# Optimization experiments

Hardware: AMD Instinct MI355X
Metric: run time of the kernel (lower is better)

Reference implementation:

```python
import jax, jax.numpy as jnp
import numpy as np


def setup_inputs() -> dict:
    key = jax.random.key(0)
    k1, k2 = jax.random.split(key)
    B, S, H, E = 4, 8192, 4096, 64
    x = jax.random.normal(k1, (B, S, H), dtype=jnp.float32)
    # gate weight [E, H], scaled like a standard init_method
    weight = jax.random.normal(k2, (E, H), dtype=jnp.float32) * (H ** -0.5)
    expert_biases = jnp.zeros((E,), dtype=jnp.float32)
    return {"x": x, "weight": weight, "expert_biases": expert_biases, "top_k": 8}


def reference(x, weight, expert_biases, top_k):
    BIAS_UPDATE_RATE = 0.01
    batch_shape = x.shape[:-1]
    E, H = weight.shape
    flat_x = x.reshape(-1, H)            # [N, H]
    n_tokens = flat_x.shape[0]

    raw_scores = flat_x @ weight.T       # [N, E] gate GEMM
    probs = jax.nn.softmax(raw_scores + expert_biases, axis=-1)  # biased softmax

    expert_weights, expert_indices = jax.lax.top_k(probs, top_k)  # [N, K]

    # bincount with fixed length E (jit-friendly scatter-add)
    token_counts = jnp.zeros((E,), jnp.int32).at[expert_indices.reshape(-1)].add(1)

    # loss-free balancing bias update (training-time buffer update)
    tokens_per_expert = n_tokens * top_k / E
    load_violations = token_counts.astype(jnp.float32) - tokens_per_expert
    new_expert_biases = expert_biases + BIAS_UPDATE_RATE * jnp.sign(load_violations)

    scores = probs.reshape(*batch_shape, E)
    expert_weights = expert_weights.reshape(*batch_shape, top_k)
    expert_indices = expert_indices.reshape(*batch_shape, top_k)
    return (scores, expert_weights, expert_indices, new_expert_biases)
```

## Files before the change

kernel.cpp:

```cpp
#include <hip/hip_runtime.h>

#define NE 64
#define TAU 1e-4f
#define LSTR 68

typedef __bf16 bf16x8 __attribute__((ext_vector_type(8)));
typedef float f32x4 __attribute__((ext_vector_type(4)));

__device__ __forceinline__ void split8(const float4 a0, const float4 a1,
                                       bf16x8& hi, bf16x8& lo) {
  const float xs[8] = {a0.x, a0.y, a0.z, a0.w, a1.x, a1.y, a1.z, a1.w};
#pragma unroll
  for (int i = 0; i < 8; ++i) {
    const __bf16 h = (__bf16)xs[i];
    hi[i] = h;
    lo[i] = (__bf16)(xs[i] - (float)h);
  }
}

__device__ __forceinline__ void gld16(const void* g, void* l) {
  __builtin_amdgcn_global_load_lds(
      (const __attribute__((address_space(1))) void*)g,
      (__attribute__((address_space(3))) void*)l, 16, 0, 0);
}

__global__ void zero512(int* __restrict__ p) { p[threadIdx.x] = 0; }

__global__ __launch_bounds__(256) void wconvert(const float* __restrict__ W,
                                                __bf16* __restrict__ Whi,
                                                __bf16* __restrict__ Wlo,
                                                int n8, int H) {
  const int i = blockIdx.x * 256 + threadIdx.x;
  if (i >= n8) return;
  const int hc = H >> 3;
  const int e = i / hc;
  const int k0 = (i - e * hc) * 8;
  const float4 a0 = *reinterpret_cast<const float4*>(W + (size_t)e * H + k0);
  const float4 a1 =
      *reinterpret_cast<const float4*>(W + (size_t)e * H + k0 + 4);
  bf16x8 hi, lo;
  split8(a0, a1, hi, lo);
  const int tt = k0 >> 5, lk = (k0 >> 3) & 3, j = e >> 4, lr = e & 15;
  const size_t off = (size_t)tt * 2048 + j * 512 + (lk * 16 + lr) * 8;
  *reinterpret_cast<bf16x8*>(Whi + off) = hi;
  *reinterpret_cast<bf16x8*>(Wlo + off) = lo;
}

template <int BUF>
__device__ __forceinline__ void issue_tile(int t, const float* const (&srcA)[4],
                                           const __bf16* srcBh,
                                           const __bf16* srcBl, char* smem,
                                           int wave) {
  float* af = (float*)(smem) + BUF * 4096;
  __bf16* bh = (__bf16*)(smem + 32768) + BUF * 4096;
  __bf16* bl = (__bf16*)(smem + 49152) + BUF * 4096;
#pragma unroll
  for (int p = 0; p < 4; ++p)
    gld16(srcA[p] + 64 * (size_t)t, af + wave * 1024 + p * 256);
  gld16(srcBh + 4096 * (size_t)t, bh + wave * 512);
  gld16(srcBh + 4096 * (size_t)t + 2048, bh + 2048 + wave * 512);
  gld16(srcBl + 4096 * (size_t)t, bl + wave * 512);
  gld16(srcBl + 4096 * (size_t)t + 2048, bl + 2048 + wave * 512);
}

template <int BUF>
__device__ __forceinline__ void compute_tile(char* smem, int wave, int lane,
                                             int lr, int lk, int swz,
                                             f32x4 (&acc)[4]) {
  const float* Aw = (float*)(smem) + BUF * 4096 + wave * 1024 + lr * 64;
  const __bf16* Bh0 = (__bf16*)(smem + 32768) + BUF * 4096;
  const __bf16* Bl0 = (__bf16*)(smem + 49152) + BUF * 4096;
#pragma unroll
  for (int kk = 0; kk < 2; ++kk) {
    const int c = 8 * kk + 2 * lk;
    const float4 f0 = *reinterpret_cast<const float4*>(Aw + 4 * (c ^ swz));
    const float4 f1 =
        *reinterpret_cast<const float4*>(Aw + 4 * ((c + 1) ^ swz));
    bf16x8 Ahi, Alo;
    split8(f0, f1, Ahi, Alo);
    const __bf16* Bh = Bh0 + kk * 2048;
    const __bf16* Bl = Bl0 + kk * 2048;
    bf16x8 BH[4], BL[4];
#pragma unroll
    for (int j = 0; j < 4; ++j) {
      BH[j] = *reinterpret_cast<const bf16x8*>(Bh + j * 512 + lane * 8);
      BL[j] = *reinterpret_cast<const bf16x8*>(Bl + j * 512 + lane * 8);
    }
#pragma unroll
    for (int j = 0; j < 4; ++j)
      acc[j] = __builtin_amdgcn_mfma_f32_16x16x32_bf16(Alo, BL[j], acc[j], 0, 0, 0);
#pragma unroll
    for (int j = 0; j < 4; ++j)
      acc[j] = __builtin_amdgcn_mfma_f32_16x16x32_bf16(Alo, BH[j], acc[j], 0, 0, 0);
#pragma unroll
    for (int j = 0; j < 4; ++j)
      acc[j] = __builtin_amdgcn_mfma_f32_16x16x32_bf16(Ahi, BL[j], acc[j], 0, 0, 0);
#pragma unroll
    for (int j = 0; j < 4; ++j)
      acc[j] = __builtin_amdgcn_mfma_f32_16x16x32_bf16(Ahi, BH[j], acc[j], 0, 0, 0);
  }
}

__global__ __launch_bounds__(256, 2) void gemm_fused(
    const float* __restrict__ X, const __bf16* __restrict__ Whi,
    const __bf16* __restrict__ Wlo, const float* __restrict__ bias,
    float* __restrict__ S, float* __restrict__ wout, float* __restrict__ iout,
    int* __restrict__ cnt, int* __restrict__ hist, int* __restrict__ list,
    int cap, int H, int K) {
  __shared__ alignas(16) char smem[65536];
  __shared__ int hist_s[NE];
  const int tid = threadIdx.x;
  const int lane = tid & 63;
  const int wave = tid >> 6;
  if (tid < NE) hist_s[tid] = 0;
  const int lr = lane & 15;
  const int lk = lane >> 4;
  const int row0 = blockIdx.x * 64;

  const float* srcA[4];
#pragma unroll
  for (int p = 0; p < 4; ++p) {
    const int rr = 4 * p + (lane >> 4);
    const int sp = lane & 15;
    srcA[p] = X + (size_t)(row0 + 16 * wave + rr) * H + 4 * (sp ^ (rr & 7));
  }
  const __bf16* srcBh = Whi + wave * 512 + lane * 8;
  const __bf16* srcBl = Wlo + wave * 512 + lane * 8;

  f32x4 acc[4] = {};
  const int T2 = H / 64;
  const int swz = lr & 7;

  issue_tile<0>(0, srcA, srcBh, srcBl, smem, wave);
  for (int t = 0; t < T2; t += 2) {
    if (t + 1 < T2) {
      issue_tile<1>(t + 1, srcA, srcBh, srcBl, smem, wave);
      asm volatile("s_waitcnt vmcnt(8)" ::: "memory");
    } else {
      asm volatile("s_waitcnt vmcnt(0)" ::: "memory");
    }
    __builtin_amdgcn_s_barrier();
    asm volatile("" ::: "memory");
    compute_tile<0>(smem, wave, lane, lr, lk, swz, acc);
    asm volatile("" ::: "memory");
    __builtin_amdgcn_s_barrier();
    asm volatile("" ::: "memory");
    if (t + 2 < T2) {
      issue_tile<0>(t + 2, srcA, srcBh, srcBl, smem, wave);
      asm volatile("s_waitcnt vmcnt(8)" ::: "memory");
    } else {
      asm volatile("s_waitcnt vmcnt(0)" ::: "memory");
    }
    __builtin_amdgcn_s_barrier();
    asm volatile("" ::: "memory");
    compute_tile<1>(smem, wave, lane, lr, lk, swz, acc);
    asm volatile("" ::: "memory");
    __builtin_amdgcn_s_barrier();
    asm volatile("" ::: "memory");
  }

  float* Ls = (float*)smem;
#pragma unroll
  for (int j = 0; j < 4; ++j)
#pragma unroll
    for (int r = 0; r < 4; ++r)
      Ls[(16 * wave + 4 * lk + r) * LSTR + 16 * j + lr] = acc[j][r];
  __syncthreads();

  const float bv = bias[lane];
  for (int tt = 0; tt < 16; ++tt) {
    const int tl = wave * 16 + tt;
    const int t = row0 + tl;
    const float s = Ls[tl * LSTR + lane] + bv;

    float m = s;
#pragma unroll
    for (int off = 32; off >= 1; off >>= 1) m = fmaxf(m, __shfl_xor(m, off));
    const float e = expf(s - m);
    float sum = e;
#pragma unroll
    for (int off = 32; off >= 1; off >>= 1) sum += __shfl_xor(sum, off);
    const float p = e / sum;

    float wsel = s;
    float rv = 0.f;
    int ri = 0;
    float prev = 0.f, mingap = 1e30f;
#pragma unroll
    for (int r = 0; r < 9; ++r) {
      float v = wsel;
      int ii = lane;
#pragma unroll
      for (int off = 32; off >= 1; off >>= 1) {
        const float ov = __shfl_xor(v, off);
        const int oi = __shfl_xor(ii, off);
        if (ov > v || (ov == v && oi < ii)) { v = ov; ii = oi; }
      }
      if (r > 0) mingap = fminf(mingap, prev - v);
      prev = v;
      const float pw = __shfl(p, ii);
      if (lane == r) { rv = pw; ri = ii; }
      if (lane == ii) wsel = -1e30f;
    }

    bool toC = false;
    if (mingap < TAU && cap > 0) {
      int pos = 0;
      if (lane == 0) pos = atomicAdd(cnt, 1);
      pos = __shfl(pos, 0);
      if (pos < cap) {
        if (lane == 0) list[pos] = t;
        toC = true;
      }
    }
    if (!toC) {
      S[(size_t)t * NE + lane] = p;
      if (lane < K) {
        wout[(size_t)t * K + lane] = rv;
        iout[(size_t)t * K + lane] = (float)ri;
        atomicAdd(&hist_s[ri], 1);
      }
    }
  }
  __syncthreads();
  if (tid < NE) atomicAdd(&hist[tid], hist_s[tid]);
}

__device__ __forceinline__ void finalize_token_f64(
    int t, int lane, double s, float* __restrict__ S, float* __restrict__ wout,
    float* __restrict__ iout, int* __restrict__ hist, int K) {
  double m = s;
#pragma unroll
  for (int off = 32; off >= 1; off >>= 1) m = fmax(m, __shfl_xor(m, off));
  const double ex = exp(s - m);
  double sum = ex;
#pragma unroll
  for (int off = 32; off >= 1; off >>= 1) sum += __shfl_xor(sum, off);
  const double p = ex / sum;
  S[(size_t)t * NE + lane] = (float)p;
  double wsel = s;
  double rv = 0.0;
  int ri = 0;
  for (int r = 0; r < K; ++r) {
    double v = wsel;
    int ii = lane;
#pragma unroll
    for (int off = 32; off >= 1; off >>= 1) {
      const double ov = __shfl_xor(v, off);
      const int oi = __shfl_xor(ii, off);
      if (ov > v || (ov == v && oi < ii)) { v = ov; ii = oi; }
    }
    const double pw = __shfl(p, ii);
    if (lane == r) { rv = pw; ri = ii; }
    if (lane == ii) wsel = -1e300;
  }
  if (lane < K) {
    wout[(size_t)t * K + lane] = (float)rv;
    iout[(size_t)t * K + lane] = (float)ri;
    atomicAdd(&hist[ri], 1);
  }
}

__global__ __launch_bounds__(256) void recompute_f64(
    const float* __restrict__ X, const float* __restrict__ W,
    const float* __restrict__ bias, float* __restrict__ S,
    float* __restrict__ wout, float* __restrict__ iout,
    const int* __restrict__ cnt, const int* __restrict__ list,
    int* __restrict__ hist, int H, int K, int cap) {
  if (cap <= 0) return;
  __shared__ float4 xs[1024];
  __shared__ double red[256];
  const int tid = threadIdx.x;
  const int n = min(*cnt, cap);
  const int H4 = H >> 2;
  for (int idx = blockIdx.x; idx < n; idx += gridDim.x) {
    const int t = list[idx];
    __syncthreads();
    const float4* xg = reinterpret_cast<const float4*>(X + (size_t)t * H);
    for (int i = tid; i < H4; i += 256) xs[i] = xg[i];
    __syncthreads();
    const int e = tid & 63, sl = tid >> 6;
    const int seg = H4 >> 2;
    const float4* wr =
        reinterpret_cast<const float4*>(W + (size_t)e * H) + (size_t)sl * seg;
    const float4* xr = &xs[sl * seg];
    double a0 = 0.0, a1 = 0.0;
    for (int k = 0; k < seg; k += 2) {
      const float4 w0 = wr[k], w1 = wr[k + 1];
      const float4 v0 = xr[k], v1 = xr[k + 1];
      a0 = fma((double)v0.x, (double)w0.x, a0);
      a0 = fma((double)v0.y, (double)w0.y, a0);
      a0 = fma((double)v0.z, (double)w0.z, a0);
      a0 = fma((double)v0.w, (double)w0.w, a0);
      a1 = fma((double)v1.x, (double)w1.x, a1);
      a1 = fma((double)v1.y, (double)w1.y, a1);
      a1 = fma((double)v1.z, (double)w1.z, a1);
      a1 = fma((double)v1.w, (double)w1.w, a1);
    }
    red[tid] = a0 + a1;
    __syncthreads();
    if (tid < 64) {
      const double s =
          red[e] + red[64 + e] + red[128 + e] + red[192 + e] + (double)bias[e];
      finalize_token_f64(t, e, s, S, wout, iout, hist, K);
    }
  }
}

__global__ void bias_update(const int* __restrict__ hist,
                            const float* __restrict__ bias,
                            float* __restrict__ bout, float tpe) {
  const int e = threadIdx.x;
  const float d = (float)hist[e] - tpe;
  const float sg = (d > 0.f) ? 1.f : ((d < 0.f) ? -1.f : 0.f);
  bout[e] = bias[e] + 0.01f * sg;
}

extern "C" void kernel_launch(void* const* d_in, const int* in_sizes, int n_in,
                              void* d_out, int out_size, void* d_ws, size_t ws_size,
                              hipStream_t stream) {
  const float* x = (const float*)d_in[0];
  const float* w = (const float*)d_in[1];
  const float* bias = (const float*)d_in[2];
  const int E = in_sizes[2];
  const int H = in_sizes[1] / E;
  const long long N = (long long)in_sizes[0] / H;
  const int K = (int)(((long long)out_size - N * E - E) / (2 * N));

  float* S = (float*)d_out;
  float* wout = S + (size_t)N * E;
  float* iout = wout + (size_t)N * K;
  float* bout = iout + (size_t)N * K;

  int* cnt = (int*)d_ws;
  int* hist = (int*)d_ws + 64;
  const size_t whalf = (size_t)E * H * sizeof(__bf16);
  __bf16* Whi = (__bf16*)((char*)d_ws + 4096);
  __bf16* Wlo = (__bf16*)((char*)d_ws + 4096 + whalf);
  const size_t listoff = 4096 + 2 * whalf;
  int* list = (int*)((char*)d_ws + listoff);
  int cap = 0;
  if (ws_size > listoff + 65536)
    cap = (int)min((size_t)32768, (ws_size - listoff) / 4);

  zero512<<<dim3(1), dim3(128), 0, stream>>>((int*)d_ws);
  const int n8 = E * H / 8;
  wconvert<<<dim3((n8 + 255) / 256), 256, 0, stream>>>(w, Whi, Wlo, n8, H);
  gemm_fused<<<dim3((int)(N / 64)), 256, 0, stream>>>(
      x, Whi, Wlo, bias, S, wout, iout, cnt, hist, list, cap, H, K);
  recompute_f64<<<dim3(512), 256, 0, stream>>>(x, w, bias, S, wout, iout, cnt,
                                               list, hist, H, K, cap);
  bias_update<<<dim3(1), dim3(E), 0, stream>>>(hist, bias, bout,
                                               (float)((double)N * K / E));
}
```

Measured before the change: 285.9 us.

## Split gate GEMM K-dimension in two and move softmax/top-k to separate kernel

```diff
diff --git a/kernel.cpp b/kernel.cpp
--- a/kernel.cpp
+++ b/kernel.cpp
@@ -47,118 +47,110 @@
 }
 
 template <int BUF>
-__device__ __forceinline__ void issue_tile(int t, const float* const (&srcA)[4],
+__device__ __forceinline__ void issue_tile(int t, const float* srcA0,
+                                           const float* srcA1,
                                            const __bf16* srcBh,
                                            const __bf16* srcBl, char* smem,
                                            int wave) {
-  float* af = (float*)(smem) + BUF * 4096;
-  __bf16* bh = (__bf16*)(smem + 32768) + BUF * 4096;
-  __bf16* bl = (__bf16*)(smem + 49152) + BUF * 4096;
-#pragma unroll
-  for (int p = 0; p < 4; ++p)
-    gld16(srcA[p] + 64 * (size_t)t, af + wave * 1024 + p * 256);
-  gld16(srcBh + 4096 * (size_t)t, bh + wave * 512);
-  gld16(srcBh + 4096 * (size_t)t + 2048, bh + 2048 + wave * 512);
-  gld16(srcBl + 4096 * (size_t)t, bl + wave * 512);
-  gld16(srcBl + 4096 * (size_t)t + 2048, bl + 2048 + wave * 512);
+  float* af = (float*)smem + BUF * 2048;
+  __bf16* bh = (__bf16*)(smem + 16384) + BUF * 2048;
+  __bf16* bl = (__bf16*)(smem + 24576) + BUF * 2048;
+  gld16(srcA0 + 32 * (size_t)t, af + wave * 512);
+  gld16(srcA1 + 32 * (size_t)t, af + wave * 512 + 256);
+  gld16(srcBh + 2048 * (size_t)t, bh + wave * 512);
+  gld16(srcBl + 2048 * (size_t)t, bl + wave * 512);
 }
 
 template <int BUF>
 __device__ __forceinline__ void compute_tile(char* smem, int wave, int lane,
-                                             int lr, int lk, int swz,
-                                             f32x4 (&acc)[4]) {
-  const float* Aw = (float*)(smem) + BUF * 4096 + wave * 1024 + lr * 64;
-  const __bf16* Bh0 = (__bf16*)(smem + 32768) + BUF * 4096;
-  const __bf16* Bl0 = (__bf16*)(smem + 49152) + BUF * 4096;
-#pragma unroll
-  for (int kk = 0; kk < 2; ++kk) {
-    const int c = 8 * kk + 2 * lk;
-    const float4 f0 = *reinterpret_cast<const float4*>(Aw + 4 * (c ^ swz));
-    const float4 f1 =
-        *reinterpret_cast<const float4*>(Aw + 4 * ((c + 1) ^ swz));
-    bf16x8 Ahi, Alo;
-    split8(f0, f1, Ahi, Alo);
-    const __bf16* Bh = Bh0 + kk * 2048;
-    const __bf16* Bl = Bl0 + kk * 2048;
-    bf16x8 BH[4], BL[4];
-#pragma unroll
-    for (int j = 0; j < 4; ++j) {
-      BH[j] = *reinterpret_cast<const bf16x8*>(Bh + j * 512 + lane * 8);
-      BL[j] = *reinterpret_cast<const bf16x8*>(Bl + j * 512 + lane * 8);
-    }
-#pragma unroll
-    for (int j = 0; j < 4; ++j)
-      acc[j] = __builtin_amdgcn_mfma_f32_16x16x32_bf16(Alo, BL[j], acc[j], 0, 0, 0);
-#pragma unroll
-    for (int j = 0; j < 4; ++j)
-      acc[j] = __builtin_amdgcn_mfma_f32_16x16x32_bf16(Alo, BH[j], acc[j], 0, 0, 0);
-#pragma unroll
-    for (int j = 0; j < 4; ++j)
-      acc[j] = __builtin_amdgcn_mfma_f32_16x16x32_bf16(Ahi, BL[j], acc[j], 0, 0, 0);
-#pragma unroll
-    for (int j = 0; j < 4; ++j)
-      acc[j] = __builtin_amdgcn_mfma_f32_16x16x32_bf16(Ahi, BH[j], acc[j], 0, 0, 0);
-  }
-}
-
-__global__ __launch_bounds__(256, 2) void gemm_fused(
+                                             int lr, int lk, f32x4 (&acc)[4]) {
+  const float* Aw = (float*)smem + BUF * 2048 + wave * 512 + (lr >> 3) * 256 +
+                    (lr & 7) * 32;
+  const int s0 = (2 * lk) ^ (lr & 7);
+  const int s1 = (2 * lk + 1) ^ (lr & 7);
+  const float4 f0 = *reinterpret_cast<const float4*>(Aw + s0 * 4);
+  const float4 f1 = *reinterpret_cast<const float4*>(Aw + s1 * 4);
+  const __bf16* Bh0 = (__bf16*)(smem + 16384) + BUF * 2048;
+  const __bf16* Bl0 = (__bf16*)(smem + 24576) + BUF * 2048;
+  bf16x8 BHf[4], BLf[4];
+#pragma unroll
+  for (int j = 0; j < 4; ++j) {
+    BHf[j] = *reinterpret_cast<const bf16x8*>(Bh0 + j * 512 + lane * 8);
+    BLf[j] = *reinterpret_cast<const bf16x8*>(Bl0 + j * 512 + lane * 8);
+  }
+  bf16x8 Ahi, Alo;
+  split8(f0, f1, Ahi, Alo);
+#pragma unroll
+  for (int j = 0; j < 4; ++j)
+    acc[j] = __builtin_amdgcn_mfma_f32_16x16x32_bf16(Alo, BLf[j], acc[j], 0, 0, 0);
+#pragma unroll
+  for (int j = 0; j < 4; ++j)
+    acc[j] = __builtin_amdgcn_mfma_f32_16x16x32_bf16(Alo, BHf[j], acc[j], 0, 0, 0);
+#pragma unroll
+  for (int j = 0; j < 4; ++j)
+    acc[j] = __builtin_amdgcn_mfma_f32_16x16x32_bf16(Ahi, BLf[j], acc[j], 0, 0, 0);
+#pragma unroll
+  for (int j = 0; j < 4; ++j)
+    acc[j] = __builtin_amdgcn_mfma_f32_16x16x32_bf16(Ahi, BHf[j], acc[j], 0, 0, 0);
+}
+
+__global__ __launch_bounds__(256, 4) void gemm_half(
     const float* __restrict__ X, const __bf16* __restrict__ Whi,
-    const __bf16* __restrict__ Wlo, const float* __restrict__ bias,
-    float* __restrict__ S, float* __restrict__ wout, float* __restrict__ iout,
-    int* __restrict__ cnt, int* __restrict__ hist, int* __restrict__ list,
-    int cap, int H, int K) {
-  __shared__ alignas(16) char smem[65536];
-  __shared__ int hist_s[NE];
+    const __bf16* __restrict__ Wlo, float* __restrict__ S0,
+    float* __restrict__ P2, int H) {
+  __shared__ alignas(16) char smem[32768];
   const int tid = threadIdx.x;
   const int lane = tid & 63;
   const int wave = tid >> 6;
-  if (tid < NE) hist_s[tid] = 0;
   const int lr = lane & 15;
   const int lk = lane >> 4;
   const int row0 = blockIdx.x * 64;
-
-  const float* srcA[4];
-#pragma unroll
-  for (int p = 0; p < 4; ++p) {
-    const int rr = 4 * p + (lane >> 4);
-    const int sp = lane & 15;
-    srcA[p] = X + (size_t)(row0 + 16 * wave + rr) * H + 4 * (sp ^ (rr & 7));
-  }
-  const __bf16* srcBh = Whi + wave * 512 + lane * 8;
-  const __bf16* srcBl = Wlo + wave * 512 + lane * 8;
+  const int kbeg = blockIdx.y * (H >> 1);
+  float* __restrict__ P = blockIdx.y ? P2 : S0;
+
+  const int rr0 = lane >> 3;
+  const int sp = lane & 7;
+  const float* srcA0 =
+      X + (size_t)(row0 + 16 * wave + rr0) * H + kbeg + 4 * (sp ^ rr0);
+  const float* srcA1 =
+      X + (size_t)(row0 + 16 * wave + 8 + rr0) * H + kbeg + 4 * (sp ^ rr0);
+  const __bf16* srcBh =
+      Whi + (size_t)(blockIdx.y * 64) * 2048 + wave * 512 + lane * 8;
+  const __bf16* srcBl =
+      Wlo + (size_t)(blockIdx.y * 64) * 2048 + wave * 512 + lane * 8;
 
   f32x4 acc[4] = {};
-  const int T2 = H / 64;
-  const int swz = lr & 7;
-
-  issue_tile<0>(0, srcA, srcBh, srcBl, smem, wave);
+  const int T2 = H >> 6;
+
+  issue_tile<0>(0, srcA0, srcA1, srcBh, srcBl, smem, wave);
   for (int t = 0; t < T2; t += 2) {
     if (t + 1 < T2) {
-      issue_tile<1>(t + 1, srcA, srcBh, srcBl, smem, wave);
-      asm volatile("s_waitcnt vmcnt(8)" ::: "memory");
+      issue_tile<1>(t + 1, srcA0, srcA1, srcBh, srcBl, smem, wave);
+      asm volatile("s_waitcnt vmcnt(4)" ::: "memory");
     } else {
       asm volatile("s_waitcnt vmcnt(0)" ::: "memory");
     }
     __builtin_amdgcn_s_barrier();
     asm volatile("" ::: "memory");
-    compute_tile<0>(smem, wave, lane, lr, lk, swz, acc);
+    compute_tile<0>(smem, wave, lane, lr, lk, acc);
     asm volatile("" ::: "memory");
     __builtin_amdgcn_s_barrier();
     asm volatile("" ::: "memory");
     if (t + 2 < T2) {
-      issue_tile<0>(t + 2, srcA, srcBh, srcBl, smem, wave);
-      asm volatile("s_waitcnt vmcnt(8)" ::: "memory");
+      issue_tile<0>(t + 2, srcA0, srcA1, srcBh, srcBl, smem, wave);
+      asm volatile("s_waitcnt vmcnt(4)" ::: "memory");
     } else {
       asm volatile("s_waitcnt vmcnt(0)" ::: "memory");
     }
     __builtin_amdgcn_s_barrier();
     asm volatile("" ::: "memory");
-    compute_tile<1>(smem, wave, lane, lr, lk, swz, acc);
+    compute_tile<1>(smem, wave, lane, lr, lk, acc);
     asm volatile("" ::: "memory");
     __builtin_amdgcn_s_barrier();
     asm volatile("" ::: "memory");
   }
 
+  __syncthreads();
   float* Ls = (float*)smem;
 #pragma unroll
   for (int j = 0; j < 4; ++j)
@@ -166,12 +158,30 @@
     for (int r = 0; r < 4; ++r)
       Ls[(16 * wave + 4 * lk + r) * LSTR + 16 * j + lr] = acc[j][r];
   __syncthreads();
-
-  const float bv = bias[lane];
   for (int tt = 0; tt < 16; ++tt) {
     const int tl = wave * 16 + tt;
-    const int t = row0 + tl;
-    const float s = Ls[tl * LSTR + lane] + bv;
+    P[(size_t)(row0 + tl) * NE + lane] = Ls[tl * LSTR + lane];
+  }
+}
+
+__global__ __launch_bounds__(256) void finish(
+    const float* __restrict__ P2, const float* __restrict__ bias,
+    float* __restrict__ S, float* __restrict__ wout, float* __restrict__ iout,
+    int* __restrict__ cnt, int* __restrict__ hist, int* __restrict__ list,
+    int cap, int K) {
+  __shared__ int hist_s[NE];
+  const int tid = threadIdx.x;
+  if (tid < NE) hist_s[tid] = 0;
+  __syncthreads();
+  const int lane = tid & 63;
+  const int wave = tid >> 6;
+  const float bv = bias[lane];
+  const int t0 = blockIdx.x * 64 + wave * 16;
+
+  for (int tt = 0; tt < 16; ++tt) {
+    const int t = t0 + tt;
+    const size_t base = (size_t)t * NE;
+    const float s = S[base + lane] + P2[base + lane] + bv;
 
     float m = s;
 #pragma unroll
@@ -214,7 +224,7 @@
       }
     }
     if (!toC) {
-      S[(size_t)t * NE + lane] = p;
+      S[base + lane] = p;
       if (lane < K) {
         wout[(size_t)t * K + lane] = rv;
         iout[(size_t)t * K + lane] = (float)ri;
@@ -337,7 +347,10 @@
   const size_t whalf = (size_t)E * H * sizeof(__bf16);
   __bf16* Whi = (__bf16*)((char*)d_ws + 4096);
   __bf16* Wlo = (__bf16*)((char*)d_ws + 4096 + whalf);
-  const size_t listoff = 4096 + 2 * whalf;
+  const size_t P2OFF = (size_t)2 << 20;
+  float* P2 = (float*)((char*)d_ws + P2OFF);
+  const size_t p2bytes = (size_t)N * NE * sizeof(float);
+  const size_t listoff = P2OFF + p2bytes;
   int* list = (int*)((char*)d_ws + listoff);
   int cap = 0;
   if (ws_size > listoff + 65536)
@@ -346,8 +359,9 @@
   zero512<<<dim3(1), dim3(128), 0, stream>>>((int*)d_ws);
   const int n8 = E * H / 8;
   wconvert<<<dim3((n8 + 255) / 256), 256, 0, stream>>>(w, Whi, Wlo, n8, H);
-  gemm_fused<<<dim3((int)(N / 64)), 256, 0, stream>>>(
-      x, Whi, Wlo, bias, S, wout, iout, cnt, hist, list, cap, H, K);
+  gemm_half<<<dim3((int)(N / 64), 2), 256, 0, stream>>>(x, Whi, Wlo, S, P2, H);
+  finish<<<dim3((int)(N / 64)), 256, 0, stream>>>(P2, bias, S, wout, iout, cnt,
+                                                  hist, list, cap, K);
   recompute_f64<<<dim3(512), 256, 0, stream>>>(x, w, bias, S, wout, iout, cnt,
                                                list, hist, H, K, cap);
   bias_update<<<dim3(1), dim3(E), 0, stream>>>(hist, bias, bout,
```

Result: slower. 299.6 us (+4.8%).
